# Kernel optimization log

Measured on AMD Instinct MI355X. Metric: run time of the kernel, lower is better.

## Reference

```python
import jax, jax.numpy as jnp
import numpy as np

N_NODES = 100000
N_EDGES = 1600000
DIM = 128
BN_EPS = 1e-5


def setup_inputs() -> dict:
    key = jax.random.key(0)
    k1, k2, k3, k4 = jax.random.split(key, 4)
    scale = 1.0 / np.sqrt(DIM)
    return {
        "x": jax.random.normal(k1, (N_NODES, DIM), dtype=jnp.float32),
        "edge_index": jax.random.randint(k2, (2, N_EDGES), 0, N_NODES, dtype=jnp.int64),
        "W_l": jax.random.normal(k3, (DIM, DIM), dtype=jnp.float32) * scale,
        "b_l": jnp.zeros((DIM,), dtype=jnp.float32),
        "W_r": jax.random.normal(k4, (DIM, DIM), dtype=jnp.float32) * scale,
        "gamma": jnp.ones((DIM,), dtype=jnp.float32),
        "beta": jnp.zeros((DIM,), dtype=jnp.float32),
    }


def reference(x, edge_index, W_l, b_l, W_r, gamma, beta):
    n = x.shape[0]
    src, dst = edge_index[0], edge_index[1]
    # SAGEConv mean aggregation: gather source features, scatter-sum to dst, divide by degree
    agg = jax.ops.segment_sum(x[src], dst, num_segments=n)          # [N, d_in]
    deg = jax.ops.segment_sum(jnp.ones_like(src, dtype=x.dtype), dst, num_segments=n)
    mean = agg / jnp.maximum(deg, 1.0)[:, None]
    # lin_l(mean) + lin_r(x)  (bias lives in lin_l, PyG default)
    h = mean @ W_l + b_l + x @ W_r                                   # [N, d_out]
    # act -> BatchNorm1d (training mode, batch stats) -> dropout(p=0, identity)
    h = jax.nn.relu(h)
    mu = jnp.mean(h, axis=0)
    var = jnp.mean(jnp.square(h - mu), axis=0)                       # biased var, as torch BN
    h = (h - mu) * jax.lax.rsqrt(var + BN_EPS) * gamma + beta
    # residual
    return x + h
```

## Files before the change

kernel.cpp:

```cpp
#include <hip/hip_runtime.h>

#define DIM 128
#define BN_EPS 1e-5f
#define NB 32
#define NBK_MAX 512

typedef __attribute__((ext_vector_type(8))) short bf16x8;
typedef __attribute__((ext_vector_type(4))) float f32x4;

union B8 { uint4 u; bf16x8 s; };

__device__ __forceinline__ ushort f2bf(float f) {
    unsigned u = __float_as_uint(f);
    u += 0x7fffu + ((u >> 16) & 1u);
    return (ushort)(u >> 16);
}

__global__ void k_prep(const float4* __restrict__ x4, const float* __restrict__ Wl,
                       const float* __restrict__ Wr, const unsigned* __restrict__ eiu,
                       int* __restrict__ bcnt, uint2* __restrict__ xf8,
                       uint4* __restrict__ xbf, uint4* __restrict__ wpack,
                       int nn, int ne, int PB, int WB) {
    __shared__ int nz;
    __shared__ int lh[NBK_MAX];
    int b = blockIdx.x;
    const int tid = threadIdx.x;

    if (b < PB) {
        const int t = b * 256 + tid;
        const int n8 = nn * DIM / 8;
        if (t < n8) {
            const float4 a = x4[2 * t], c = x4[2 * t + 1];
            int u0 = __builtin_amdgcn_cvt_pk_fp8_f32(a.x, a.y, 0, false);
            u0 = __builtin_amdgcn_cvt_pk_fp8_f32(a.z, a.w, u0, true);
            int u1 = __builtin_amdgcn_cvt_pk_fp8_f32(c.x, c.y, 0, false);
            u1 = __builtin_amdgcn_cvt_pk_fp8_f32(c.z, c.w, u1, true);
            xf8[t] = make_uint2((unsigned)u0, (unsigned)u1);
            uint4 xb;
            xb.x = ((unsigned)f2bf(a.y) << 16) | f2bf(a.x);
            xb.y = ((unsigned)f2bf(a.w) << 16) | f2bf(a.z);
            xb.z = ((unsigned)f2bf(c.y) << 16) | f2bf(c.x);
            xb.w = ((unsigned)f2bf(c.w) << 16) | f2bf(c.z);
            xbf[t] = xb;
        }
        return;
    }
    b -= PB;
    if (b < WB) {
        const int t = b * 256 + tid;
        const int lane = t & 63, kk = (t >> 6) & 3, nt = (t >> 8) & 7, mat = t >> 11;
        const float* W = mat ? Wr : Wl;
        const int k0 = kk * 32 + (lane >> 4) * 8;
        const int n = nt * 16 + (lane & 15);
        ushort e[8];
#pragma unroll
        for (int j = 0; j < 8; ++j) e[j] = f2bf(W[(size_t)(k0 + j) * DIM + n]);
        uint4 o;
        o.x = ((unsigned)e[1] << 16) | e[0];
        o.y = ((unsigned)e[3] << 16) | e[2];
        o.z = ((unsigned)e[5] << 16) | e[4];
        o.w = ((unsigned)e[7] << 16) | e[6];
        wpack[t] = o;
        return;
    }
    b -= WB;
    const int nbk = (nn + 255) >> 8;
    for (int i = tid; i < nbk; i += 256) lh[i] = 0;
    if (tid == 0) nz = 0;
    __syncthreads();
    const int e0 = b * 4096;
    {
        int es = e0 + tid * 16;
        if (es >= ne) es = ne - 1;
        if (eiu[2 * (size_t)es + 1] != 0) atomicOr(&nz, 1);
    }
    __syncthreads();
    const int is64 = (nz == 0);
    for (int j = 0; j < 16; ++j) {
        const int e = e0 + j * 256 + tid;
        if (e < ne) {
            int dst;
            if (is64) dst = (int)((const long long*)eiu)[(size_t)ne + e];
            else      dst = ((const int*)eiu)[(size_t)ne + e];
            atomicAdd(&lh[dst >> 8], 1);
        }
    }
    __syncthreads();
    for (int i = tid; i < nbk; i += 256)
        if (lh[i]) atomicAdd(&bcnt[i], lh[i]);
}

__global__ __launch_bounds__(512) void k_scanb(const int* __restrict__ bcnt,
                                               int* __restrict__ bbase,
                                               int* __restrict__ cursor2, int nn, int ne) {
    __shared__ int sd[512];
    const int nbk = (nn + 255) >> 8;
    const int tid = threadIdx.x;
    const int v = (tid < nbk) ? bcnt[tid] : 0;
    sd[tid] = v;
    __syncthreads();
    for (int ofs = 1; ofs < 512; ofs <<= 1) {
        const int t = (tid >= ofs) ? sd[tid - ofs] : 0;
        __syncthreads();
        sd[tid] += t;
        __syncthreads();
    }
    if (tid < nbk) {
        const int ex = sd[tid] - v;
        bbase[tid] = ex;
        cursor2[tid] = ex;
    }
    if (tid == 0) bbase[nbk] = ne;
}

__global__ __launch_bounds__(256) void k_passA(const unsigned* __restrict__ eiu,
                                               int* __restrict__ cursor2,
                                               unsigned* __restrict__ pairbuf,
                                               int nn, int ne) {
    __shared__ int lh[NBK_MAX];
    __shared__ int gb[NBK_MAX];
    __shared__ int nz;
    const int nbk = (nn + 255) >> 8;
    const int tid = threadIdx.x;
    const int e0 = blockIdx.x * 4096;
    for (int i = tid; i < nbk; i += 256) lh[i] = 0;
    if (tid == 0) nz = 0;
    __syncthreads();
    {
        int es = e0 + tid * 16;
        if (es >= ne) es = ne - 1;
        if (eiu[2 * (size_t)es + 1] != 0) atomicOr(&nz, 1);
    }
    __syncthreads();
    const int is64 = (nz == 0);
    unsigned pay[16];
    int bkrank[16];
#pragma unroll
    for (int j = 0; j < 16; ++j) {
        const int e = e0 + j * 256 + tid;
        bkrank[j] = -1;
        if (e < ne) {
            int src, dst;
            if (is64) {
                const long long* p = (const long long*)eiu;
                src = (int)p[e];
                dst = (int)p[(size_t)ne + e];
            } else {
                const int* p = (const int*)eiu;
                src = p[e];
                dst = p[(size_t)ne + e];
            }
            const int bk = dst >> 8;
            const int rank = atomicAdd(&lh[bk], 1);
            bkrank[j] = (bk << 16) | rank;
            pay[j] = ((unsigned)(dst & 255) << 24) | (unsigned)src;
        }
    }
    __syncthreads();
    for (int i = tid; i < nbk; i += 256) {
        const int c = lh[i];
        gb[i] = c ? atomicAdd(&cursor2[i], c) : 0;
    }
    __syncthreads();
#pragma unroll
    for (int j = 0; j < 16; ++j) {
        if (bkrank[j] >= 0) {
            const int bk = bkrank[j] >> 16, rank = bkrank[j] & 0xFFFF;
            pairbuf[gb[bk] + rank] = pay[j];
        }
    }
}

__global__ __launch_bounds__(256) void k_passB(const unsigned* __restrict__ pairbuf,
                                               const int* __restrict__ bbase,
                                               int* __restrict__ off, int* __restrict__ cnt,
                                               int* __restrict__ srcbuf, int nn) {
    __shared__ int cl[256];
    __shared__ int sd[256];
    __shared__ int cur[256];
    const int tid = threadIdx.x;
    const int b = blockIdx.x;
    const int node0 = b << 8;
    const int e0 = bbase[b], e1 = bbase[b + 1];
    cl[tid] = 0;
    __syncthreads();
    for (int e = e0 + tid; e < e1; e += 256)
        atomicAdd(&cl[pairbuf[e] >> 24], 1);
    __syncthreads();
    const int v = cl[tid];
    sd[tid] = v;
    __syncthreads();
    for (int ofs = 1; ofs < 256; ofs <<= 1) {
        const int t = (tid >= ofs) ? sd[tid - ofs] : 0;
        __syncthreads();
        sd[tid] += t;
        __syncthreads();
    }
    const int ex = sd[tid] - v;
    cur[tid] = ex;
    const int node = node0 + tid;
    if (node < nn) {
        off[node] = e0 + ex;
        cnt[node] = v;
    }
    __syncthreads();
    for (int e = e0 + tid; e < e1; e += 256) {
        const unsigned p = pairbuf[e];
        const int pos = atomicAdd(&cur[p >> 24], 1);
        srcbuf[e0 + pos] = (int)(p & 0xFFFFFFu);
    }
}

__global__ __launch_bounds__(512, 4) void k_gemm(
    const uint4* __restrict__ xbf, const uint2* __restrict__ xf8,
    const uint4* __restrict__ wpack, const float* __restrict__ bl,
    const int* __restrict__ off, const int* __restrict__ cnt,
    const int* __restrict__ srcbuf,
    ushort* __restrict__ hout, float* __restrict__ ssum, float* __restrict__ ssq,
    int nn)
{
    __shared__ uint4 mean4[NB * 16];
    __shared__ uint4 xls4[NB * 16];
    __shared__ float red_sum[2][DIM];
    __shared__ float red_sq[2][DIM];

    const int tid = threadIdx.x;
    const int lane = tid & 63;
    const int w = tid >> 6;
    const int base = blockIdx.x * NB;
    const int q = lane & 15;

#define CVT8(v)                                                           \
    {                                                                     \
        auto p0 = __builtin_amdgcn_cvt_pk_f32_fp8((v).x, false);          \
        auto p1 = __builtin_amdgcn_cvt_pk_f32_fp8((v).x, true);           \
        auto p2 = __builtin_amdgcn_cvt_pk_f32_fp8((v).y, false);          \
        auto p3 = __builtin_amdgcn_cvt_pk_f32_fp8((v).y, true);           \
        acc[0] += p0[0]; acc[1] += p0[1]; acc[2] += p1[0]; acc[3] += p1[1]; \
        acc[4] += p2[0]; acc[5] += p2[1]; acc[6] += p3[0]; acc[7] += p3[1]; \
    }

    {
        const int ln = w * 4 + (lane >> 4);
        const int node = base + ln;
        float acc[8];
#pragma unroll
        for (int j = 0; j < 8; ++j) acc[j] = 0.f;
        uint4 xp = make_uint4(0, 0, 0, 0);

        if (node < nn) {
            xp = xbf[(size_t)node * 16 + q];

            const int o = off[node];
            const int c = cnt[node];
            int e = 0;
            for (; e + 8 <= c; e += 8) {
                const int s0 = srcbuf[o + e + 0];
                const int s1 = srcbuf[o + e + 1];
                const int s2 = srcbuf[o + e + 2];
                const int s3 = srcbuf[o + e + 3];
                const int s4 = srcbuf[o + e + 4];
                const int s5 = srcbuf[o + e + 5];
                const int s6 = srcbuf[o + e + 6];
                const int s7 = srcbuf[o + e + 7];
                const uint2 v0 = xf8[(size_t)s0 * 16 + q];
                const uint2 v1 = xf8[(size_t)s1 * 16 + q];
                const uint2 v2 = xf8[(size_t)s2 * 16 + q];
                const uint2 v3 = xf8[(size_t)s3 * 16 + q];
                const uint2 v4 = xf8[(size_t)s4 * 16 + q];
                const uint2 v5 = xf8[(size_t)s5 * 16 + q];
                const uint2 v6 = xf8[(size_t)s6 * 16 + q];
                const uint2 v7 = xf8[(size_t)s7 * 16 + q];
                CVT8(v0); CVT8(v1); CVT8(v2); CVT8(v3);
                CVT8(v4); CVT8(v5); CVT8(v6); CVT8(v7);
            }
            for (; e + 4 <= c; e += 4) {
                const int s0 = srcbuf[o + e + 0];
                const int s1 = srcbuf[o + e + 1];
                const int s2 = srcbuf[o + e + 2];
                const int s3 = srcbuf[o + e + 3];
                const uint2 v0 = xf8[(size_t)s0 * 16 + q];
                const uint2 v1 = xf8[(size_t)s1 * 16 + q];
                const uint2 v2 = xf8[(size_t)s2 * 16 + q];
                const uint2 v3 = xf8[(size_t)s3 * 16 + q];
                CVT8(v0); CVT8(v1); CVT8(v2); CVT8(v3);
            }
            for (; e < c; ++e) {
                const int s = srcbuf[o + e];
                const uint2 v = xf8[(size_t)s * 16 + q];
                CVT8(v);
            }
            const float r = 1.0f / fmaxf((float)c, 1.0f);
#pragma unroll
            for (int j = 0; j < 8; ++j) acc[j] *= r;
        }
#undef CVT8

        const int slot = q ^ (ln & 15);
        xls4[ln * 16 + slot] = xp;
        uint4 mp;
        mp.x = ((unsigned)f2bf(acc[1]) << 16) | f2bf(acc[0]);
        mp.y = ((unsigned)f2bf(acc[3]) << 16) | f2bf(acc[2]);
        mp.z = ((unsigned)f2bf(acc[5]) << 16) | f2bf(acc[4]);
        mp.w = ((unsigned)f2bf(acc[7]) << 16) | f2bf(acc[6]);
        mean4[ln * 16 + slot] = mp;
    }
    __syncthreads();

    const int m = w & 1;
    const int nh = w >> 1;
    const int row16 = lane & 15;
    const int kgrp = lane >> 4;
    const int ln2 = m * 16 + row16;

    bf16x8 am[4], ax[4];
#pragma unroll
    for (int kk = 0; kk < 4; ++kk) {
        const int unit = (kk * 4 + kgrp) ^ row16;
        B8 va, vb;
        va.u = mean4[ln2 * 16 + unit];
        vb.u = xls4[ln2 * 16 + unit];
        am[kk] = va.s;
        ax[kk] = vb.s;
    }

    f32x4 acc2[2];
#pragma unroll
    for (int j = 0; j < 2; ++j) {
        const float bv = bl[(nh * 2 + j) * 16 + row16];
        acc2[j] = (f32x4){bv, bv, bv, bv};
    }

#pragma unroll
    for (int j = 0; j < 2; ++j) {
        const int nt = nh * 2 + j;
        const uint4* pl = wpack + (size_t)(nt * 4) * 64 + lane;
        const uint4* pr = wpack + (size_t)((8 + nt) * 4) * 64 + lane;
        B8 wl[4], wr[4];
#pragma unroll
        for (int kk = 0; kk < 4; ++kk) {
            wl[kk].u = pl[kk * 64];
            wr[kk].u = pr[kk * 64];
        }
#pragma unroll
        for (int kk = 0; kk < 4; ++kk)
            acc2[j] = __builtin_amdgcn_mfma_f32_16x16x32_bf16(am[kk], wl[kk].s, acc2[j], 0, 0, 0);
#pragma unroll
        for (int kk = 0; kk < 4; ++kk)
            acc2[j] = __builtin_amdgcn_mfma_f32_16x16x32_bf16(ax[kk], wr[kk].s, acc2[j], 0, 0, 0);
    }

#pragma unroll
    for (int j = 0; j < 2; ++j) {
        const int feat = (nh * 2 + j) * 16 + row16;
        float s = 0.f, sq = 0.f;
#pragma unroll
        for (int r = 0; r < 4; ++r) {
            const int node = base + m * 16 + kgrp * 4 + r;
            const float v = fmaxf(acc2[j][r], 0.0f);
            if (node < nn) {
                hout[(size_t)node * DIM + feat] = f2bf(v);
                s += v;
                sq += v * v;
            }
        }
        s += __shfl_xor(s, 16);
        s += __shfl_xor(s, 32);
        sq += __shfl_xor(sq, 16);
        sq += __shfl_xor(sq, 32);
        if (lane < 16) {
            red_sum[m][feat] = s;
            red_sq[m][feat] = sq;
        }
    }
    __syncthreads();
    if (tid < DIM) {
        atomicAdd(&ssum[tid], red_sum[0][tid] + red_sum[1][tid]);
        atomicAdd(&ssq[tid], red_sq[0][tid] + red_sq[1][tid]);
    }
}

__global__ __launch_bounds__(512) void k_finalize(
    const uint4* __restrict__ xbf, const uint4* __restrict__ h4,
    const float* __restrict__ ssum, const float* __restrict__ ssq,
    const float* __restrict__ gamma, const float* __restrict__ beta,
    float4* __restrict__ out4, int nn)
{
    const float invN = 1.0f / (float)nn;
    const int tid = threadIdx.x;
    const int node = blockIdx.x * 32 + (tid >> 4);
    const int q = tid & 15;
    if (node >= nn) return;
    const uint4 hv = h4[(size_t)node * 16 + q];
    const uint4 xv = xbf[(size_t)node * 16 + q];
    const float4 s4a = ((const float4*)ssum)[2 * q], s4b = ((const float4*)ssum)[2 * q + 1];
    const float4 q4a = ((const float4*)ssq)[2 * q], q4b = ((const float4*)ssq)[2 * q + 1];
    const float4 g4a = ((const float4*)gamma)[2 * q], g4b = ((const float4*)gamma)[2 * q + 1];
    const float4 b4a = ((const float4*)beta)[2 * q], b4b = ((const float4*)beta)[2 * q + 1];
    float h[8], x[8];
    h[0] = __uint_as_float(hv.x << 16);
    h[1] = __uint_as_float(hv.x & 0xffff0000u);
    h[2] = __uint_as_float(hv.y << 16);
    h[3] = __uint_as_float(hv.y & 0xffff0000u);
    h[4] = __uint_as_float(hv.z << 16);
    h[5] = __uint_as_float(hv.z & 0xffff0000u);
    h[6] = __uint_as_float(hv.w << 16);
    h[7] = __uint_as_float(hv.w & 0xffff0000u);
    x[0] = __uint_as_float(xv.x << 16);
    x[1] = __uint_as_float(xv.x & 0xffff0000u);
    x[2] = __uint_as_float(xv.y << 16);
    x[3] = __uint_as_float(xv.y & 0xffff0000u);
    x[4] = __uint_as_float(xv.z << 16);
    x[5] = __uint_as_float(xv.z & 0xffff0000u);
    x[6] = __uint_as_float(xv.w << 16);
    x[7] = __uint_as_float(xv.w & 0xffff0000u);
    float4 oa, ob;
    {
        const float mu = s4a.x * invN, rs = rsqrtf(q4a.x * invN - mu * mu + BN_EPS);
        oa.x = x[0] + (h[0] - mu) * rs * g4a.x + b4a.x;
    }
    {
        const float mu = s4a.y * invN, rs = rsqrtf(q4a.y * invN - mu * mu + BN_EPS);
        oa.y = x[1] + (h[1] - mu) * rs * g4a.y + b4a.y;
    }
    {
        const float mu = s4a.z * invN, rs = rsqrtf(q4a.z * invN - mu * mu + BN_EPS);
        oa.z = x[2] + (h[2] - mu) * rs * g4a.z + b4a.z;
    }
    {
        const float mu = s4a.w * invN, rs = rsqrtf(q4a.w * invN - mu * mu + BN_EPS);
        oa.w = x[3] + (h[3] - mu) * rs * g4a.w + b4a.w;
    }
    {
        const float mu = s4b.x * invN, rs = rsqrtf(q4b.x * invN - mu * mu + BN_EPS);
        ob.x = x[4] + (h[4] - mu) * rs * g4b.x + b4b.x;
    }
    {
        const float mu = s4b.y * invN, rs = rsqrtf(q4b.y * invN - mu * mu + BN_EPS);
        ob.y = x[5] + (h[5] - mu) * rs * g4b.y + b4b.y;
    }
    {
        const float mu = s4b.z * invN, rs = rsqrtf(q4b.z * invN - mu * mu + BN_EPS);
        ob.z = x[6] + (h[6] - mu) * rs * g4b.z + b4b.z;
    }
    {
        const float mu = s4b.w * invN, rs = rsqrtf(q4b.w * invN - mu * mu + BN_EPS);
        ob.w = x[7] + (h[7] - mu) * rs * g4b.w + b4b.w;
    }
    out4[(size_t)node * 32 + 2 * q] = oa;
    out4[(size_t)node * 32 + 2 * q + 1] = ob;
}

extern "C" void kernel_launch(void* const* d_in, const int* in_sizes, int n_in,
                              void* d_out, int out_size, void* d_ws, size_t ws_size,
                              hipStream_t stream) {
    const float* x     = (const float*)d_in[0];
    const void*  ei    = d_in[1];
    const float* Wl    = (const float*)d_in[2];
    const float* bl    = (const float*)d_in[3];
    const float* Wr    = (const float*)d_in[4];
    const float* gamma = (const float*)d_in[5];
    const float* beta  = (const float*)d_in[6];
    float* out = (float*)d_out;

    const int nn = in_sizes[0] / DIM;
    const int ne = in_sizes[1] / 2;
    const int nbk = (nn + 255) >> 8;

    int* ws = (int*)d_ws;
    int*   bcnt    = ws;
    float* ssum    = (float*)(ws + 512);
    float* ssq     = (float*)(ws + 640);
    int*   bbase   = ws + 768;
    int*   cursor2 = ws + 1280;
    int*   cnt     = ws + 1792;
    int*   off     = cnt + nn;
    size_t pos = 1792 + 2 * (size_t)nn;
    pos = (pos + 3) & ~(size_t)3;
    uint4* wpack  = (uint4*)(ws + pos);
    int*   srcbuf = (int*)(wpack + 4096);
    size_t p2 = (size_t)(srcbuf + ne - ws);
    p2 = (p2 + 3) & ~(size_t)3;
    uint2* xf8 = (uint2*)(ws + p2);
    unsigned* pairbuf = (unsigned*)(xf8 + (size_t)nn * 16);
    ushort*   hbuf    = (ushort*)pairbuf;
    uint4*    xbf     = (uint4*)(hbuf + (size_t)nn * DIM);

    hipMemsetAsync(d_ws, 0, 768 * sizeof(int), stream);

    const int PB = (nn * DIM / 8 + 255) / 256;
    const int WB = 16;
    const int HB = (ne + 4095) / 4096;
    k_prep<<<PB + WB + HB, 256, 0, stream>>>((const float4*)x, Wl, Wr,
                                             (const unsigned*)ei, bcnt, xf8, xbf, wpack,
                                             nn, ne, PB, WB);
    k_scanb<<<1, 512, 0, stream>>>(bcnt, bbase, cursor2, nn, ne);
    k_passA<<<(ne + 4095) / 4096, 256, 0, stream>>>((const unsigned*)ei, cursor2,
                                                    pairbuf, nn, ne);
    k_passB<<<nbk, 256, 0, stream>>>(pairbuf, bbase, off, cnt, srcbuf, nn);
    const int ntile = (nn + NB - 1) / NB;
    k_gemm<<<ntile, 512, 0, stream>>>(xbf, xf8, wpack, bl,
                                      off, cnt, srcbuf, hbuf, ssum, ssq, nn);
    k_finalize<<<ntile, 512, 0, stream>>>(xbf, (const uint4*)hbuf,
                                          ssum, ssq, gamma, beta, (float4*)out, nn);
}
```

Baseline: 184.4 us.

## Shrink gemm tiles to 16 nodes, software-pipeline gathers, pack offset/count

Halves the k_gemm tile to 16 nodes with 256-thread blocks, so each of four waves computes two column tiles for all 16 rows and the two-way M split and its reduction go away. The neighbour gather loop is software-pipelined: the next batch of eight fp8 rows is loaded while the previous batch is converted and accumulated, aiming to hide gather latency. Offset and count per node are packed into one int2 so a single load replaces two. Smaller blocks double the block count and the number of stat atomics, and the double buffer adds register pressure.

```diff
diff --git a/kernel.cpp b/kernel.cpp
--- a/kernel.cpp
+++ b/kernel.cpp
@@ -2,7 +2,7 @@
 
 #define DIM 128
 #define BN_EPS 1e-5f
-#define NB 32
+#define NB 16
 #define NBK_MAX 512
 
 typedef __attribute__((ext_vector_type(8))) short bf16x8;
@@ -173,7 +173,7 @@
 
 __global__ __launch_bounds__(256) void k_passB(const unsigned* __restrict__ pairbuf,
                                                const int* __restrict__ bbase,
-                                               int* __restrict__ off, int* __restrict__ cnt,
+                                               int2* __restrict__ off2,
                                                int* __restrict__ srcbuf, int nn) {
     __shared__ int cl[256];
     __shared__ int sd[256];
@@ -199,10 +199,7 @@
     const int ex = sd[tid] - v;
     cur[tid] = ex;
     const int node = node0 + tid;
-    if (node < nn) {
-        off[node] = e0 + ex;
-        cnt[node] = v;
-    }
+    if (node < nn) off2[node] = make_int2(e0 + ex, v);
     __syncthreads();
     for (int e = e0 + tid; e < e1; e += 256) {
         const unsigned p = pairbuf[e];
@@ -211,18 +208,17 @@
     }
 }
 
-__global__ __launch_bounds__(512, 4) void k_gemm(
+__global__ __launch_bounds__(256, 8) void k_gemm(
     const uint4* __restrict__ xbf, const uint2* __restrict__ xf8,
     const uint4* __restrict__ wpack, const float* __restrict__ bl,
-    const int* __restrict__ off, const int* __restrict__ cnt,
-    const int* __restrict__ srcbuf,
+    const int2* __restrict__ off2, const int* __restrict__ srcbuf,
     ushort* __restrict__ hout, float* __restrict__ ssum, float* __restrict__ ssq,
     int nn)
 {
     __shared__ uint4 mean4[NB * 16];
     __shared__ uint4 xls4[NB * 16];
-    __shared__ float red_sum[2][DIM];
-    __shared__ float red_sq[2][DIM];
+    __shared__ float red_sum[DIM];
+    __shared__ float red_sq[DIM];
 
     const int tid = threadIdx.x;
     const int lane = tid & 63;
@@ -243,61 +239,56 @@
     {
         const int ln = w * 4 + (lane >> 4);
         const int node = base + ln;
+        const int slot = q ^ (ln & 15);
         float acc[8];
 #pragma unroll
         for (int j = 0; j < 8; ++j) acc[j] = 0.f;
-        uint4 xp = make_uint4(0, 0, 0, 0);
+        int o = 0, c = 0;
 
         if (node < nn) {
-            xp = xbf[(size_t)node * 16 + q];
-
-            const int o = off[node];
-            const int c = cnt[node];
-            int e = 0;
-            for (; e + 8 <= c; e += 8) {
-                const int s0 = srcbuf[o + e + 0];
-                const int s1 = srcbuf[o + e + 1];
-                const int s2 = srcbuf[o + e + 2];
-                const int s3 = srcbuf[o + e + 3];
-                const int s4 = srcbuf[o + e + 4];
-                const int s5 = srcbuf[o + e + 5];
-                const int s6 = srcbuf[o + e + 6];
-                const int s7 = srcbuf[o + e + 7];
-                const uint2 v0 = xf8[(size_t)s0 * 16 + q];
-                const uint2 v1 = xf8[(size_t)s1 * 16 + q];
-                const uint2 v2 = xf8[(size_t)s2 * 16 + q];
-                const uint2 v3 = xf8[(size_t)s3 * 16 + q];
-                const uint2 v4 = xf8[(size_t)s4 * 16 + q];
-                const uint2 v5 = xf8[(size_t)s5 * 16 + q];
-                const uint2 v6 = xf8[(size_t)s6 * 16 + q];
-                const uint2 v7 = xf8[(size_t)s7 * 16 + q];
-                CVT8(v0); CVT8(v1); CVT8(v2); CVT8(v3);
-                CVT8(v4); CVT8(v5); CVT8(v6); CVT8(v7);
+            xls4[ln * 16 + slot] = xbf[(size_t)node * 16 + q];
+            const int2 oc = off2[node];
+            o = oc.x;
+            c = oc.y;
+        } else {
+            xls4[ln * 16 + slot] = make_uint4(0, 0, 0, 0);
+        }
+
+        const int* sp = srcbuf + o;
+        int e = 0;
+        if (c >= 8) {
+            uint2 va[8];
+            {
+                int s[8];
+#pragma unroll
+                for (int j = 0; j < 8; ++j) s[j] = sp[j];
+#pragma unroll
+                for (int j = 0; j < 8; ++j) va[j] = xf8[(size_t)s[j] * 16 + q];
             }
-            for (; e + 4 <= c; e += 4) {
-                const int s0 = srcbuf[o + e + 0];
-                const int s1 = srcbuf[o + e + 1];
-                const int s2 = srcbuf[o + e + 2];
-                const int s3 = srcbuf[o + e + 3];
-                const uint2 v0 = xf8[(size_t)s0 * 16 + q];
-                const uint2 v1 = xf8[(size_t)s1 * 16 + q];
-                const uint2 v2 = xf8[(size_t)s2 * 16 + q];
-                const uint2 v3 = xf8[(size_t)s3 * 16 + q];
-                CVT8(v0); CVT8(v1); CVT8(v2); CVT8(v3);
+            for (e = 8; e + 8 <= c; e += 8) {
+                int sb[8];
+#pragma unroll
+                for (int j = 0; j < 8; ++j) sb[j] = sp[e + j];
+                uint2 vb[8];
+#pragma unroll
+                for (int j = 0; j < 8; ++j) vb[j] = xf8[(size_t)sb[j] * 16 + q];
+#pragma unroll
+                for (int j = 0; j < 8; ++j) CVT8(va[j]);
+#pragma unroll
+                for (int j = 0; j < 8; ++j) va[j] = vb[j];
             }
-            for (; e < c; ++e) {
-                const int s = srcbuf[o + e];
-                const uint2 v = xf8[(size_t)s * 16 + q];
-                CVT8(v);
-            }
-            const float r = 1.0f / fmaxf((float)c, 1.0f);
-#pragma unroll
-            for (int j = 0; j < 8; ++j) acc[j] *= r;
-        }
+#pragma unroll
+            for (int j = 0; j < 8; ++j) CVT8(va[j]);
+        }
+        for (; e < c; ++e) {
+            const uint2 v = xf8[(size_t)sp[e] * 16 + q];
+            CVT8(v);
+        }
+        const float r = 1.0f / fmaxf((float)c, 1.0f);
+#pragma unroll
+        for (int j = 0; j < 8; ++j) acc[j] *= r;
 #undef CVT8
 
-        const int slot = q ^ (ln & 15);
-        xls4[ln * 16 + slot] = xp;
         uint4 mp;
         mp.x = ((unsigned)f2bf(acc[1]) << 16) | f2bf(acc[0]);
         mp.y = ((unsigned)f2bf(acc[3]) << 16) | f2bf(acc[2]);
@@ -307,19 +298,16 @@
     }
     __syncthreads();
 
-    const int m = w & 1;
-    const int nh = w >> 1;
     const int row16 = lane & 15;
     const int kgrp = lane >> 4;
-    const int ln2 = m * 16 + row16;
 
     bf16x8 am[4], ax[4];
 #pragma unroll
     for (int kk = 0; kk < 4; ++kk) {
         const int unit = (kk * 4 + kgrp) ^ row16;
         B8 va, vb;
-        va.u = mean4[ln2 * 16 + unit];
-        vb.u = xls4[ln2 * 16 + unit];
+        va.u = mean4[row16 * 16 + unit];
+        vb.u = xls4[row16 * 16 + unit];
         am[kk] = va.s;
         ax[kk] = vb.s;
     }
@@ -327,13 +315,13 @@
     f32x4 acc2[2];
 #pragma unroll
     for (int j = 0; j < 2; ++j) {
-        const float bv = bl[(nh * 2 + j) * 16 + row16];
+        const float bv = bl[(w * 2 + j) * 16 + row16];
         acc2[j] = (f32x4){bv, bv, bv, bv};
     }
 
 #pragma unroll
     for (int j = 0; j < 2; ++j) {
-        const int nt = nh * 2 + j;
+        const int nt = w * 2 + j;
         const uint4* pl = wpack + (size_t)(nt * 4) * 64 + lane;
         const uint4* pr = wpack + (size_t)((8 + nt) * 4) * 64 + lane;
         B8 wl[4], wr[4];
@@ -352,11 +340,11 @@
 
 #pragma unroll
     for (int j = 0; j < 2; ++j) {
-        const int feat = (nh * 2 + j) * 16 + row16;
+        const int feat = (w * 2 + j) * 16 + row16;
         float s = 0.f, sq = 0.f;
 #pragma unroll
         for (int r = 0; r < 4; ++r) {
-            const int node = base + m * 16 + kgrp * 4 + r;
+            const int node = base + kgrp * 4 + r;
             const float v = fmaxf(acc2[j][r], 0.0f);
             if (node < nn) {
                 hout[(size_t)node * DIM + feat] = f2bf(v);
@@ -369,14 +357,14 @@
         sq += __shfl_xor(sq, 16);
         sq += __shfl_xor(sq, 32);
         if (lane < 16) {
-            red_sum[m][feat] = s;
-            red_sq[m][feat] = sq;
+            red_sum[feat] = s;
+            red_sq[feat] = sq;
         }
     }
     __syncthreads();
     if (tid < DIM) {
-        atomicAdd(&ssum[tid], red_sum[0][tid] + red_sum[1][tid]);
-        atomicAdd(&ssq[tid], red_sq[0][tid] + red_sq[1][tid]);
+        atomicAdd(&ssum[tid], red_sum[tid]);
+        atomicAdd(&ssq[tid], red_sq[tid]);
     }
 }
 
@@ -473,8 +461,7 @@
     float* ssq     = (float*)(ws + 640);
     int*   bbase   = ws + 768;
     int*   cursor2 = ws + 1280;
-    int*   cnt     = ws + 1792;
-    int*   off     = cnt + nn;
+    int2*  off2    = (int2*)(ws + 1792);
     size_t pos = 1792 + 2 * (size_t)nn;
     pos = (pos + 3) & ~(size_t)3;
     uint4* wpack  = (uint4*)(ws + pos);
@@ -497,10 +484,11 @@
     k_scanb<<<1, 512, 0, stream>>>(bcnt, bbase, cursor2, nn, ne);
     k_passA<<<(ne + 4095) / 4096, 256, 0, stream>>>((const unsigned*)ei, cursor2,
                                                     pairbuf, nn, ne);
-    k_passB<<<nbk, 256, 0, stream>>>(pairbuf, bbase, off, cnt, srcbuf, nn);
+    k_passB<<<nbk, 256, 0, stream>>>(pairbuf, bbase, off2, srcbuf, nn);
     const int ntile = (nn + NB - 1) / NB;
-    k_gemm<<<ntile, 512, 0, stream>>>(xbf, xf8, wpack, bl,
-                                      off, cnt, srcbuf, hbuf, ssum, ssq, nn);
-    k_finalize<<<ntile, 512, 0, stream>>>(xbf, (const uint4*)hbuf,
-                                          ssum, ssq, gamma, beta, (float4*)out, nn);
-}
+    k_gemm<<<ntile, 256, 0, stream>>>(xbf, xf8, wpack, bl,
+                                      off2, srcbuf, hbuf, ssum, ssq, nn);
+    k_finalize<<<(nn + 31) / 32, 512, 0, stream>>>(xbf, (const uint4*)hbuf,
+                                                   ssum, ssq, gamma, beta,
+                                                   (float4*)out, nn);
+}
```

Result: slower. 262.1 us (+42.1%).
